# Kernel optimization log

Measured on AMD Instinct MI355X. Metric: run time of the kernel, lower is better.

## Reference

```python
import jax, jax.numpy as jnp
import numpy as np

VOCAB = 50000
EMB = 256
HID = 256
MAX_PRED = 30
B = 64
S_ENC = 100


def setup_inputs() -> dict:
    key = jax.random.key(0)
    ks = jax.random.split(key, 16)
    s = 1.0 / np.sqrt(HID)
    return {
        "comment": jax.random.randint(ks[0], (B, 29), 0, VOCAB),
        "comment_input": jax.random.randint(ks[1], (B, 30), 0, VOCAB),
        "tok_output": jax.random.normal(ks[2], (B, S_ENC, HID), jnp.float32),
        "tok_enc_hc": jax.random.normal(ks[3], (1, B, HID), jnp.float32),
        "sbtao_output": jax.random.normal(ks[4], (B, S_ENC, HID), jnp.float32),
        "wemb": jax.random.normal(ks[5], (VOCAB, EMB), jnp.float32) * 0.02,
        "W_ih": jax.random.uniform(ks[6], (3 * HID, EMB), jnp.float32, -s, s),
        "W_hh": jax.random.uniform(ks[7], (3 * HID, HID), jnp.float32, -s, s),
        "b_ih": jax.random.uniform(ks[8], (3 * HID,), jnp.float32, -s, s),
        "b_hh": jax.random.uniform(ks[9], (3 * HID,), jnp.float32, -s, s),
        "W1": jax.random.uniform(ks[10], (HID, 3 * HID), jnp.float32, -s, s),
        "b1": jax.random.uniform(ks[11], (HID,), jnp.float32, -s, s),
        "W2": jax.random.uniform(ks[12], (VOCAB, HID), jnp.float32, -s, s),
        "b2": jax.random.uniform(ks[13], (VOCAB,), jnp.float32, -s, s),
    }


def _decode(comment_input, T, tok_output, h0, sbtao_output,
            wemb, W_ih, W_hh, b_ih, b_hh, W1, b1, W2, b2):
    # h0: [B,H]. The torch code re-uses hidden=tok_enc_hc at EVERY step,
    # so each step is an independent GRU-cell step -> vectorize over T.
    bsz = comment_input.shape[0]
    H = h0.shape[-1]
    emb = wemb[comment_input[:, :T]]                      # [B,T,E]
    gi = emb @ W_ih.T + b_ih                              # [B,T,3H]
    gh = h0 @ W_hh.T + b_hh                               # [B,3H]
    gh = gh[:, None, :]                                   # broadcast over T
    r = jax.nn.sigmoid(gi[..., :H] + gh[..., :H])
    z = jax.nn.sigmoid(gi[..., H:2 * H] + gh[..., H:2 * H])
    n = jnp.tanh(gi[..., 2 * H:] + r * gh[..., 2 * H:])
    dec = (1.0 - z) * n + z * h0[:, None, :]              # [B,T,H]

    def attend(enc):  # enc: [B,S,H]
        S = enc.shape[1]
        # Faithful to torch: keys come from a RESHAPE [B,S,H] -> [B,H,S]
        # (memory reinterpretation), not a transpose.
        keys = enc.reshape(bsz, H, S)
        a = jax.nn.softmax(jnp.einsum('bth,bhs->bts', dec, keys), axis=-1)
        return jnp.einsum('bts,bsh->bth', a, enc)         # [B,T,H]

    ctx = attend(tok_output)
    ast_ctx = attend(sbtao_output)
    cat = jnp.concatenate([ctx, dec, ast_ctx], axis=-1)   # [B,T,3H]
    out = jax.nn.relu(cat @ W1.T + b1)                    # [B,T,H]
    out = jax.nn.relu(out @ W2.T + b2)                    # [B,T,V]
    logprobs = jax.nn.log_softmax(out, axis=-1)           # [B,T,V]
    return logprobs


def reference(comment, comment_input, tok_output, tok_enc_hc, sbtao_output,
              wemb, W_ih, W_hh, b_ih, b_hh, W1, b1, W2, b2):
    T = min(comment.shape[1] + 1, MAX_PRED)
    h0 = tok_enc_hc[0]
    logprobs = _decode(comment_input, T, tok_output, h0, sbtao_output,
                       wemb, W_ih, W_hh, b_ih, b_hh, W1, b1, W2, b2)
    seq = jnp.argmax(logprobs, axis=-1).astype(jnp.int64 if jax.config.jax_enable_x64 else jnp.int32)
    return seq, logprobs
```

## Files before the change

### kernel.cpp

```cpp
#include <hip/hip_runtime.h>
#include <hip/hip_bf16.h>
#include <math.h>

#define NROW 1920
#define VOCAB_ 50000
#define NPAD 50048
#define NBLK 391
#define CAP 128

typedef __attribute__((ext_vector_type(8))) short short8;
typedef __attribute__((ext_vector_type(4))) float floatx4;

__device__ inline ushort f32_to_bf16_bits(float f) {
    union { float f; unsigned u; } v; v.f = f;
    unsigned u = v.u;
    u += 0x7fffu + ((u >> 16) & 1u);
    return (ushort)(u >> 16);
}

__global__ __launch_bounds__(256) void front_gemm_kernel(
    const float* __restrict__ h0, const float* __restrict__ W_hh,
    const float* __restrict__ b_hh, float* __restrict__ gh,
    const int* __restrict__ tokens, const float* __restrict__ wemb,
    const float* __restrict__ W_ih, const float* __restrict__ b_ih,
    float* __restrict__ gi) {
    __shared__ float As[32][68];
    __shared__ float Bs[32][68];
    __shared__ int tok_s[64];

    const int tid = threadIdx.x;
    const int bid = blockIdx.x;
    const bool is_gh = (bid < 12);

    int m0, n0;
    const float* Bm;
    const float* bias;
    float* C;
    if (is_gh) {
        m0 = 0; n0 = bid * 64; Bm = W_hh; bias = b_hh; C = gh;
    } else {
        int bb = bid - 12;
        m0 = (bb / 12) * 64; n0 = (bb % 12) * 64;
        Bm = W_ih; bias = b_ih; C = gi;
    }

    if (!is_gh && tid < 64) tok_s[tid] = tokens[m0 + tid];
    __syncthreads();

    const int tx = tid & 15;
    const int ty = tid >> 4;
    const int lrow = tid >> 3;
    const int lcol = (tid & 7) * 4;

    float acc[4][4];
#pragma unroll
    for (int i = 0; i < 4; ++i)
#pragma unroll
        for (int j = 0; j < 4; ++j) acc[i][j] = 0.f;

    for (int k0 = 0; k0 < 256; k0 += 32) {
#pragma unroll
        for (int half = 0; half < 2; ++half) {
            int m = lrow + half * 32;
            const float* arow = is_gh ? (h0 + (size_t)(m0 + m) * 256)
                                      : (wemb + (size_t)tok_s[m] * 256);
            float4 av = *reinterpret_cast<const float4*>(arow + k0 + lcol);
            As[lcol + 0][m] = av.x; As[lcol + 1][m] = av.y;
            As[lcol + 2][m] = av.z; As[lcol + 3][m] = av.w;
            int n = lrow + half * 32;
            float4 bv = *reinterpret_cast<const float4*>(
                Bm + (size_t)(n0 + n) * 256 + k0 + lcol);
            Bs[lcol + 0][n] = bv.x; Bs[lcol + 1][n] = bv.y;
            Bs[lcol + 2][n] = bv.z; Bs[lcol + 3][n] = bv.w;
        }
        __syncthreads();
#pragma unroll
        for (int k = 0; k < 32; ++k) {
            float4 a4 = *reinterpret_cast<const float4*>(&As[k][ty * 4]);
            float4 b4 = *reinterpret_cast<const float4*>(&Bs[k][tx * 4]);
            float a[4] = {a4.x, a4.y, a4.z, a4.w};
            float b[4] = {b4.x, b4.y, b4.z, b4.w};
#pragma unroll
            for (int i = 0; i < 4; ++i)
#pragma unroll
                for (int j = 0; j < 4; ++j) acc[i][j] = fmaf(a[i], b[j], acc[i][j]);
        }
        __syncthreads();
    }
#pragma unroll
    for (int i = 0; i < 4; ++i) {
        int m = m0 + ty * 4 + i;
#pragma unroll
        for (int j = 0; j < 4; ++j) {
            int n = n0 + tx * 4 + j;
            C[(size_t)m * 768 + n] = acc[i][j] + bias[n];
        }
    }
}

__global__ void conv_w2_kernel(const float* __restrict__ W2, ushort* __restrict__ Wb) {
    int row = blockIdx.x;
    int col = threadIdx.x;
    float v = (row < VOCAB_) ? W2[(size_t)row * 256 + col] : 0.f;
    Wb[(size_t)row * 256 + col] = f32_to_bf16_bits(v);
}

__global__ __launch_bounds__(256) void dec_attn_kernel(
    const float* __restrict__ gi, const float* __restrict__ gh,
    const float* __restrict__ h0, const float* __restrict__ tok_output,
    const float* __restrict__ sbtao, float* __restrict__ cat) {
    __shared__ float decs[256];
    __shared__ float sc[100];
    __shared__ float redbuf[128];

    int n = blockIdx.x;
    int b = n / 30;
    int tid = threadIdx.x;

    float gir = gi[(size_t)n * 768 + tid];
    float giz = gi[(size_t)n * 768 + 256 + tid];
    float gin = gi[(size_t)n * 768 + 512 + tid];
    float ghr = gh[(size_t)b * 768 + tid];
    float ghz = gh[(size_t)b * 768 + 256 + tid];
    float ghn = gh[(size_t)b * 768 + 512 + tid];
    float r = 1.f / (1.f + expf(-(gir + ghr)));
    float z = 1.f / (1.f + expf(-(giz + ghz)));
    float nnv = tanhf(gin + r * ghn);
    float d = (1.f - z) * nnv + z * h0[(size_t)b * 256 + tid];
    decs[tid] = d;
    cat[(size_t)n * 768 + 256 + tid] = d;
    __syncthreads();

    for (int a = 0; a < 2; ++a) {
        const float* e = (a == 0 ? tok_output : sbtao) + (size_t)b * 25600;
        int colbase = (a == 0) ? 0 : 512;
        if (tid < 100) {
            float acc = 0.f;
            for (int h = 0; h < 256; ++h)
                acc = fmaf(decs[h], e[h * 100 + tid], acc);
            sc[tid] = acc;
        }
        __syncthreads();
        if (tid < 128) redbuf[tid] = (tid < 100) ? sc[tid] : -1e30f;
        __syncthreads();
        for (int off = 64; off > 0; off >>= 1) {
            if (tid < off) redbuf[tid] = fmaxf(redbuf[tid], redbuf[tid + off]);
            __syncthreads();
        }
        float mx = redbuf[0];
        __syncthreads();
        if (tid < 100) sc[tid] = expf(sc[tid] - mx);
        __syncthreads();
        if (tid < 128) redbuf[tid] = (tid < 100) ? sc[tid] : 0.f;
        __syncthreads();
        for (int off = 64; off > 0; off >>= 1) {
            if (tid < off) redbuf[tid] += redbuf[tid + off];
            __syncthreads();
        }
        float inv = 1.f / redbuf[0];
        __syncthreads();
        float acc = 0.f;
        for (int s = 0; s < 100; ++s)
            acc = fmaf(sc[s], e[(size_t)s * 256 + tid], acc);
        cat[(size_t)n * 768 + colbase + tid] = acc * inv;
        __syncthreads();
    }
}

template <bool RELU>
__global__ __launch_bounds__(256) void gemm_nt_kernel(
    const float* __restrict__ A, const float* __restrict__ Bm,
    const float* __restrict__ bias, float* __restrict__ C,
    ushort* __restrict__ Cbf,
    int M, int N, int K) {
    __shared__ float As[32][68];
    __shared__ float Bs[32][68];

    const int tid = threadIdx.x;
    const int m0 = blockIdx.y * 64;
    const int n0 = blockIdx.x * 64;
    const int tx = tid & 15;
    const int ty = tid >> 4;
    const int lrow = tid >> 3;
    const int lcol = (tid & 7) * 4;

    float acc[4][4];
#pragma unroll
    for (int i = 0; i < 4; ++i)
#pragma unroll
        for (int j = 0; j < 4; ++j) acc[i][j] = 0.f;

    for (int k0 = 0; k0 < K; k0 += 32) {
#pragma unroll
        for (int half = 0; half < 2; ++half) {
            int m = lrow + half * 32;
            float4 av = *reinterpret_cast<const float4*>(
                A + (size_t)(m0 + m) * K + k0 + lcol);
            As[lcol + 0][m] = av.x; As[lcol + 1][m] = av.y;
            As[lcol + 2][m] = av.z; As[lcol + 3][m] = av.w;
            int n = lrow + half * 32;
            float4 bv = make_float4(0.f, 0.f, 0.f, 0.f);
            if (n0 + n < N)
                bv = *reinterpret_cast<const float4*>(
                    Bm + (size_t)(n0 + n) * K + k0 + lcol);
            Bs[lcol + 0][n] = bv.x; Bs[lcol + 1][n] = bv.y;
            Bs[lcol + 2][n] = bv.z; Bs[lcol + 3][n] = bv.w;
        }
        __syncthreads();
#pragma unroll
        for (int k = 0; k < 32; ++k) {
            float4 a4 = *reinterpret_cast<const float4*>(&As[k][ty * 4]);
            float4 b4 = *reinterpret_cast<const float4*>(&Bs[k][tx * 4]);
            float a[4] = {a4.x, a4.y, a4.z, a4.w};
            float b[4] = {b4.x, b4.y, b4.z, b4.w};
#pragma unroll
            for (int i = 0; i < 4; ++i)
#pragma unroll
                for (int j = 0; j < 4; ++j) acc[i][j] = fmaf(a[i], b[j], acc[i][j]);
        }
        __syncthreads();
    }
#pragma unroll
    for (int i = 0; i < 4; ++i) {
        int m = m0 + ty * 4 + i;
#pragma unroll
        for (int j = 0; j < 4; ++j) {
            int n = n0 + tx * 4 + j;
            if (n < N) {
                float v = acc[i][j] + bias[n];
                if (RELU) v = fmaxf(v, 0.f);
                C[(size_t)m * N + n] = v;
                if (Cbf) Cbf[(size_t)m * N + n] = f32_to_bf16_bits(v);
            }
        }
    }
}

template <int MODE>
__global__ __launch_bounds__(256) void mfma_gemm_kernel(
    const ushort* __restrict__ Abf, const ushort* __restrict__ Bbf,
    const float* __restrict__ b2, float* __restrict__ C,
    float* __restrict__ pmax, float* __restrict__ psum,
    const float* __restrict__ row_max, const float* __restrict__ row_lse,
    int* __restrict__ cnt, int* __restrict__ cand) {
    __shared__ ushort As[128 * 64];
    __shared__ ushort Bs[128 * 64];
    __shared__ float pmL[128][2];
    __shared__ float psL[128][2];

    const int tid = threadIdx.x;
    const int m0 = blockIdx.x * 128;
    const int n0 = blockIdx.y * 128;
    const int nblk = blockIdx.y;
    const int wave = tid >> 6, lane = tid & 63;
    const int wm = wave >> 1, wn = wave & 1;
    const int q = lane >> 4, ln = lane & 15;

    const int lrow = lane >> 3;
    const int lcol8 = (lane & 7) * 8;

    floatx4 acc[4][4];
#pragma unroll
    for (int i = 0; i < 4; ++i)
#pragma unroll
        for (int j = 0; j < 4; ++j) acc[i][j] = (floatx4)0.f;

    for (int k0 = 0; k0 < 256; k0 += 64) {
        __syncthreads();
#pragma unroll
        for (int c = 0; c < 4; ++c) {
            int rbase = wave * 32 + c * 8;
            const ushort* ga = Abf + (size_t)(m0 + rbase + lrow) * 256 + k0 + lcol8;
            const ushort* gb = Bbf + (size_t)(n0 + rbase + lrow) * 256 + k0 + lcol8;
            __builtin_amdgcn_global_load_lds(
                (const __attribute__((address_space(1))) unsigned int*)ga,
                (__attribute__((address_space(3))) unsigned int*)&As[rbase * 64],
                16, 0, 0);
            __builtin_amdgcn_global_load_lds(
                (const __attribute__((address_space(1))) unsigned int*)gb,
                (__attribute__((address_space(3))) unsigned int*)&Bs[rbase * 64],
                16, 0, 0);
        }
        __syncthreads();
#pragma unroll
        for (int ks = 0; ks < 2; ++ks) {
            short8 af[4], bf[4];
#pragma unroll
            for (int mt = 0; mt < 4; ++mt)
                af[mt] = *reinterpret_cast<const short8*>(
                    &As[(wm * 64 + mt * 16 + ln) * 64 + ks * 32 + q * 8]);
#pragma unroll
            for (int nt = 0; nt < 4; ++nt)
                bf[nt] = *reinterpret_cast<const short8*>(
                    &Bs[(wn * 64 + nt * 16 + ln) * 64 + ks * 32 + q * 8]);
#pragma unroll
            for (int mt = 0; mt < 4; ++mt)
#pragma unroll
                for (int nt = 0; nt < 4; ++nt)
                    acc[mt][nt] = __builtin_amdgcn_mfma_f32_16x16x32_bf16(
                        af[mt], bf[nt], acc[mt][nt], 0, 0, 0);
        }
    }

    float bias[4]; int nn[4];
#pragma unroll
    for (int nt = 0; nt < 4; ++nt) {
        int n = n0 + wn * 64 + nt * 16 + ln;
        nn[nt] = n;
        bias[nt] = (n < VOCAB_) ? b2[n] : 0.f;
    }

    if (MODE == 0) {
#pragma unroll
        for (int mt = 0; mt < 4; ++mt) {
#pragma unroll
            for (int r = 0; r < 4; ++r) {
                float vv[4]; float lmax = -1e30f;
#pragma unroll
                for (int nt = 0; nt < 4; ++nt) {
                    float v = acc[mt][nt][r] + bias[nt];
                    v = fmaxf(v, 0.f);
                    if (nn[nt] >= VOCAB_) v = -1e30f;
                    vv[nt] = v;
                    lmax = fmaxf(lmax, v);
                }
#pragma unroll
                for (int off = 1; off < 16; off <<= 1)
                    lmax = fmaxf(lmax, __shfl_xor(lmax, off, 64));
                float ls = 0.f;
#pragma unroll
                for (int nt = 0; nt < 4; ++nt) ls += __expf(vv[nt] - lmax);
#pragma unroll
                for (int off = 1; off < 16; off <<= 1)
                    ls += __shfl_xor(ls, off, 64);
                if (ln == 0) {
                    int rl = wm * 64 + mt * 16 + q * 4 + r;
                    pmL[rl][wn] = lmax;
                    psL[rl][wn] = ls;
                }
            }
        }
        __syncthreads();
        if (tid < 128) {
            float m1 = pmL[tid][0], m2 = pmL[tid][1];
            float nm = fmaxf(m1, m2);
            float s = psL[tid][0] * __expf(m1 - nm) + psL[tid][1] * __expf(m2 - nm);
            pmax[(size_t)(m0 + tid) * NBLK + nblk] = nm;
            psum[(size_t)(m0 + tid) * NBLK + nblk] = s;
        }
    } else {
#pragma unroll
        for (int mt = 0; mt < 4; ++mt) {
#pragma unroll
            for (int r = 0; r < 4; ++r) {
                int m = m0 + wm * 64 + mt * 16 + q * 4 + r;
                float thr = row_max[m] - 0.03f;
                float rl = row_lse[m];
#pragma unroll
                for (int nt = 0; nt < 4; ++nt) {
                    if (nn[nt] < VOCAB_) {
                        float v = acc[mt][nt][r] + bias[nt];
                        v = fmaxf(v, 0.f);
                        C[(size_t)m * VOCAB_ + nn[nt]] = v - rl;
                        if (v >= thr) {
                            int k = atomicAdd(&cnt[m], 1);
                            if (k < CAP) cand[m * CAP + k] = nn[nt];
                        }
                    }
                }
            }
        }
    }
}

__global__ __launch_bounds__(128) void reduce_rows_kernel(
    const float* __restrict__ pmax, const float* __restrict__ psum,
    float* __restrict__ row_max, float* __restrict__ row_lse,
    int* __restrict__ cnt) {
    __shared__ float sm[128], ss[128];
    int row = blockIdx.x, tid = threadIdx.x;
    if (tid == 0) cnt[row] = 0;
    const float* pm = pmax + (size_t)row * NBLK;
    const float* ps = psum + (size_t)row * NBLK;
    float m = -1e30f, s = 0.f;
    for (int i = tid; i < NBLK; i += 128) {
        float m2 = pm[i], s2 = ps[i];
        float nm = fmaxf(m, m2);
        s = s * __expf(m - nm) + s2 * __expf(m2 - nm);
        m = nm;
    }
    sm[tid] = m; ss[tid] = s;
    __syncthreads();
    for (int off = 64; off > 0; off >>= 1) {
        if (tid < off) {
            float m2 = sm[tid + off], s2 = ss[tid + off];
            float nm = fmaxf(sm[tid], m2);
            ss[tid] = ss[tid] * __expf(sm[tid] - nm) + s2 * __expf(m2 - nm);
            sm[tid] = nm;
        }
        __syncthreads();
    }
    if (tid == 0) {
        row_max[row] = sm[0];
        row_lse[row] = sm[0] + logf(ss[0]);
    }
}

__global__ __launch_bounds__(256) void final_cand_kernel(
    const int* __restrict__ cnt, const int* __restrict__ cand,
    const float* __restrict__ out1, const float* __restrict__ W2,
    const float* __restrict__ b2, float* __restrict__ seq) {
    __shared__ float o1s[256];
    __shared__ double red[256];
    __shared__ double bestv_s;
    __shared__ int besti_s;

    int row = blockIdx.x, tid = threadIdx.x;
    if (tid == 0) { bestv_s = -1e300; besti_s = 0x7fffffff; }
    o1s[tid] = out1[(size_t)row * 256 + tid];
    __syncthreads();

    int nc = min(cnt[row], CAP);
    for (int j = 0; j < nc; ++j) {
        int c = cand[row * CAP + j];
        red[tid] = (double)o1s[tid] * (double)W2[(size_t)c * 256 + tid];
        __syncthreads();
        for (int off = 128; off > 0; off >>= 1) {
            if (tid < off) red[tid] += red[tid + off];
            __syncthreads();
        }
        if (tid == 0) {
            double v = red[0] + (double)b2[c];
            if (v < 0.0) v = 0.0;
            if (v > bestv_s || (v == bestv_s && c < besti_s)) { bestv_s = v; besti_s = c; }
        }
        __syncthreads();
    }
    if (tid == 0) seq[row] = (float)(besti_s == 0x7fffffff ? 0 : besti_s);
}

extern "C" void kernel_launch(void* const* d_in, const int* in_sizes, int n_in,
                              void* d_out, int out_size, void* d_ws, size_t ws_size,
                              hipStream_t stream) {
    const int* comment_input = (const int*)d_in[1];
    const float* tok_output  = (const float*)d_in[2];
    const float* h0          = (const float*)d_in[3];
    const float* sbtao       = (const float*)d_in[4];
    const float* wemb        = (const float*)d_in[5];
    const float* W_ih        = (const float*)d_in[6];
    const float* W_hh        = (const float*)d_in[7];
    const float* b_ih        = (const float*)d_in[8];
    const float* b_hh        = (const float*)d_in[9];
    const float* W1          = (const float*)d_in[10];
    const float* b1          = (const float*)d_in[11];
    const float* W2          = (const float*)d_in[12];
    const float* b2          = (const float*)d_in[13];

    float* out    = (float*)d_out;
    float* seq    = out;
    float* logits = out + NROW;

    float* ws      = (float*)d_ws;
    float* scratch = ws;
    float* gi      = scratch + 491520;
    float* gh      = gi + 1474560;
    float* cat     = gh + 49152;
    float* out1    = cat + 1474560;
    float* pmax    = out1 + 491520;
    float* psum    = pmax + 750720;
    float* row_max = psum + 750720;
    float* row_lse = row_max + 1920;
    ushort* out1b  = (ushort*)(row_lse + 1920);
    ushort* W2b    = (ushort*)(row_lse + 1920 + 245760);
    int* cnt       = (int*)scratch;
    int* cand      = cnt + 1920;

    front_gemm_kernel<<<372, 256, 0, stream>>>(
        h0, W_hh, b_hh, gh, comment_input, wemb, W_ih, b_ih, gi);

    conv_w2_kernel<<<NPAD, 256, 0, stream>>>(W2, W2b);

    dec_attn_kernel<<<NROW, 256, 0, stream>>>(
        gi, gh, h0, tok_output, sbtao, cat);

    gemm_nt_kernel<true><<<dim3(4, 30), 256, 0, stream>>>(
        cat, W1, b1, out1, out1b, NROW, 256, 768);

    mfma_gemm_kernel<0><<<dim3(15, NBLK), 256, 0, stream>>>(
        out1b, W2b, b2, logits, pmax, psum, nullptr, nullptr, nullptr, nullptr);

    reduce_rows_kernel<<<NROW, 128, 0, stream>>>(pmax, psum, row_max, row_lse, cnt);

    mfma_gemm_kernel<1><<<dim3(15, NBLK), 256, 0, stream>>>(
        out1b, W2b, b2, logits, nullptr, nullptr, row_max, row_lse, cnt, cand);

    final_cand_kernel<<<NROW, 256, 0, stream>>>(
        cnt, cand, out1, W2, b2, seq);
}
```

Before: 845.6 us.

## Load full K tile into LDS once in MFMA GEMM; split attention score dot over two halves

The MFMA vocab GEMM now stages the entire K=256 slice of A and B (128x256 bf16 each) into shared memory in a single pass instead of four 64-wide K chunks, which removes the per-chunk barriers and lets all loads be in flight together. This raises LDS use to about 128KB per block, which can cut occupancy to one block per CU and removes any overlap between loading and compute across K steps. Separately, the attention score loop in the decoder kernel uses 200 threads, each summing half of the hidden dimension, combined through an extra shared buffer and barrier, to shorten the serial dot-product chain.

```diff
diff --git a/kernel.cpp b/kernel.cpp
--- a/kernel.cpp
+++ b/kernel.cpp
@@ -110,6 +110,7 @@
     const float* __restrict__ h0, const float* __restrict__ tok_output,
     const float* __restrict__ sbtao, float* __restrict__ cat) {
     __shared__ float decs[256];
+    __shared__ float par[2][100];
     __shared__ float sc[100];
     __shared__ float redbuf[128];
 
@@ -134,12 +135,18 @@
     for (int a = 0; a < 2; ++a) {
         const float* e = (a == 0 ? tok_output : sbtao) + (size_t)b * 25600;
         int colbase = (a == 0) ? 0 : 512;
-        if (tid < 100) {
+        if (tid < 200) {
+            int half = (tid >= 100) ? 1 : 0;
+            int s = tid - half * 100;
             float acc = 0.f;
-            for (int h = 0; h < 256; ++h)
-                acc = fmaf(decs[h], e[h * 100 + tid], acc);
-            sc[tid] = acc;
-        }
+            for (int h = 0; h < 128; ++h) {
+                int hh = half * 128 + h;
+                acc = fmaf(decs[hh], e[hh * 100 + s], acc);
+            }
+            par[half][s] = acc;
+        }
+        __syncthreads();
+        if (tid < 100) sc[tid] = par[0][tid] + par[1][tid];
         __syncthreads();
         if (tid < 128) redbuf[tid] = (tid < 100) ? sc[tid] : -1e30f;
         __syncthreads();
@@ -243,8 +250,8 @@
     float* __restrict__ pmax, float* __restrict__ psum,
     const float* __restrict__ row_max, const float* __restrict__ row_lse,
     int* __restrict__ cnt, int* __restrict__ cand) {
-    __shared__ ushort As[128 * 64];
-    __shared__ ushort Bs[128 * 64];
+    __shared__ ushort As[128 * 256];
+    __shared__ ushort Bs[128 * 256];
     __shared__ float pmL[128][2];
     __shared__ float psL[128][2];
 
@@ -256,8 +263,24 @@
     const int wm = wave >> 1, wn = wave & 1;
     const int q = lane >> 4, ln = lane & 15;
 
-    const int lrow = lane >> 3;
-    const int lcol8 = (lane & 7) * 8;
+    const int srow_off = lane >> 5;
+    const int sce = (lane & 31) * 8;
+
+#pragma unroll
+    for (int i = 0; i < 16; ++i) {
+        int rbase = wave * 32 + i * 2;
+        const ushort* ga = Abf + (size_t)(m0 + rbase + srow_off) * 256 + sce;
+        const ushort* gb = Bbf + (size_t)(n0 + rbase + srow_off) * 256 + sce;
+        __builtin_amdgcn_global_load_lds(
+            (const __attribute__((address_space(1))) unsigned int*)ga,
+            (__attribute__((address_space(3))) unsigned int*)&As[rbase * 256],
+            16, 0, 0);
+        __builtin_amdgcn_global_load_lds(
+            (const __attribute__((address_space(1))) unsigned int*)gb,
+            (__attribute__((address_space(3))) unsigned int*)&Bs[rbase * 256],
+            16, 0, 0);
+    }
+    __syncthreads();
 
     floatx4 acc[4][4];
 #pragma unroll
@@ -265,41 +288,23 @@
 #pragma unroll
         for (int j = 0; j < 4; ++j) acc[i][j] = (floatx4)0.f;
 
-    for (int k0 = 0; k0 < 256; k0 += 64) {
-        __syncthreads();
-#pragma unroll
-        for (int c = 0; c < 4; ++c) {
-            int rbase = wave * 32 + c * 8;
-            const ushort* ga = Abf + (size_t)(m0 + rbase + lrow) * 256 + k0 + lcol8;
-            const ushort* gb = Bbf + (size_t)(n0 + rbase + lrow) * 256 + k0 + lcol8;
-            __builtin_amdgcn_global_load_lds(
-                (const __attribute__((address_space(1))) unsigned int*)ga,
-                (__attribute__((address_space(3))) unsigned int*)&As[rbase * 64],
-                16, 0, 0);
-            __builtin_amdgcn_global_load_lds(
-                (const __attribute__((address_space(1))) unsigned int*)gb,
-                (__attribute__((address_space(3))) unsigned int*)&Bs[rbase * 64],
-                16, 0, 0);
-        }
-        __syncthreads();
-#pragma unroll
-        for (int ks = 0; ks < 2; ++ks) {
-            short8 af[4], bf[4];
-#pragma unroll
-            for (int mt = 0; mt < 4; ++mt)
-                af[mt] = *reinterpret_cast<const short8*>(
-                    &As[(wm * 64 + mt * 16 + ln) * 64 + ks * 32 + q * 8]);
+#pragma unroll
+    for (int kk = 0; kk < 8; ++kk) {
+        short8 af[4], bfr[4];
+#pragma unroll
+        for (int mt = 0; mt < 4; ++mt)
+            af[mt] = *reinterpret_cast<const short8*>(
+                &As[(wm * 64 + mt * 16 + ln) * 256 + kk * 32 + q * 8]);
+#pragma unroll
+        for (int nt = 0; nt < 4; ++nt)
+            bfr[nt] = *reinterpret_cast<const short8*>(
+                &Bs[(wn * 64 + nt * 16 + ln) * 256 + kk * 32 + q * 8]);
+#pragma unroll
+        for (int mt = 0; mt < 4; ++mt)
 #pragma unroll
             for (int nt = 0; nt < 4; ++nt)
-                bf[nt] = *reinterpret_cast<const short8*>(
-                    &Bs[(wn * 64 + nt * 16 + ln) * 64 + ks * 32 + q * 8]);
-#pragma unroll
-            for (int mt = 0; mt < 4; ++mt)
-#pragma unroll
-                for (int nt = 0; nt < 4; ++nt)
-                    acc[mt][nt] = __builtin_amdgcn_mfma_f32_16x16x32_bf16(
-                        af[mt], bf[nt], acc[mt][nt], 0, 0, 0);
-        }
+                acc[mt][nt] = __builtin_amdgcn_mfma_f32_16x16x32_bf16(
+                    af[mt], bfr[nt], acc[mt][nt], 0, 0, 0);
     }
 
     float bias[4]; int nn[4];
```

Result: slower. 1.169 ms (+38.3%).
